# Kernel tuning notes

Measured on AMD Instinct MI355X. Metric: run time of the kernel, lower is better.

The kernel has to match this reference:

```python
import math
import jax, jax.numpy as jnp
import numpy as np

B, S, H, NH = 2, 2048, 1024, 16
HD = H // NH
SQRT7 = math.sqrt(7.0)


def bitlinear(x, W, scale):
    # ternary weight quant: round(W / mean|W|) clipped to [-1,1], rescaled
    w_mean = jnp.mean(jnp.abs(W))
    w_q = jnp.clip(jnp.round(W / (w_mean + 1e-5)), -1.0, 1.0)
    return x @ (w_q * w_mean * scale).T


def int4_quant(x):
    beta = jnp.mean(jnp.abs(x), axis=-1, keepdims=True)
    scale = beta * SQRT7
    x_q = jnp.clip(jnp.round(x * SQRT7 / (beta + 1e-5)), -8.0, 7.0)
    return x_q * scale / SQRT7


def int8_quant(x):
    gamma = jnp.max(jnp.abs(x), axis=-1, keepdims=True)
    x_q = jnp.clip(jnp.round(x * 127.0 / (gamma + 1e-5)), -128.0, 127.0)
    return x_q * gamma / 127.0


def topk_sparsify(x, k_frac=0.5):
    abs_x = jnp.abs(x)
    num_keep = int(k_frac * x.shape[-1])
    # torch.kthvalue(k=num_keep) -> num_keep-th smallest (1-indexed)
    sorted_abs = jnp.sort(abs_x, axis=-1)
    threshold = sorted_abs[..., num_keep - 1:num_keep]
    mask = (abs_x >= threshold).astype(x.dtype)
    return x * mask


def setup_inputs() -> dict:
    key = jax.random.key(0)
    ks = jax.random.split(key, 5)
    inp = {
        "hidden_states": jax.random.normal(ks[0], (B, S, H), dtype=jnp.float32),
        "Wq": jax.random.normal(ks[1], (H, H), dtype=jnp.float32) * (1.0 / math.sqrt(H)),
        "Wk": jax.random.normal(ks[2], (H, H), dtype=jnp.float32) * (1.0 / math.sqrt(H)),
        "Wv": jax.random.normal(ks[3], (H, H), dtype=jnp.float32) * (1.0 / math.sqrt(H)),
        "Wo": jax.random.normal(ks[4], (H, H), dtype=jnp.float32) * (1.0 / math.sqrt(H)),
        "sq": jnp.ones((1,), dtype=jnp.float32),
        "sk": jnp.ones((1,), dtype=jnp.float32),
        "sv": jnp.ones((1,), dtype=jnp.float32),
        "so": jnp.ones((1,), dtype=jnp.float32),
    }
    return inp


def reference(hidden_states, Wq, Wk, Wv, Wo, sq, sk, sv, so):
    x = int4_quant(hidden_states)                      # [B,S,H]
    q = bitlinear(x, Wq, sq).reshape(B, S, NH, HD)
    k = bitlinear(x, Wk, sk).reshape(B, S, NH, HD)
    v = bitlinear(x, Wv, sv).reshape(B, S, NH, HD)
    scores = jnp.einsum("bqhd,bkhd->bhqk", q, k) / math.sqrt(HD)
    probs = jax.nn.softmax(scores, axis=-1)
    ctx = jnp.einsum("bhqk,bkhd->bqhd", probs, v).reshape(B, S, H)
    ctx = int8_quant(ctx)
    ctx = topk_sparsify(ctx, 0.5)
    return bitlinear(ctx, Wo, so)
```

## Files before the change

### kernel.cpp

```cpp
#include <hip/hip_runtime.h>
#include <math.h>

#define NTOK 4096
#define HDIM 1024
#define NHEADS 16
#define HD 64
#define SEQ 2048
#define WSZ (HDIM*HDIM)
#define NM (NTOK*HDIM)
#define SQ7F 2.6457513110645906f
#define KC_BLK 384


__global__ __launch_bounds__(1024) void k_wmean_s1(const float* __restrict__ Wq,
                                                   const float* __restrict__ Wk,
                                                   const float* __restrict__ Wv,
                                                   const float* __restrict__ Wo,
                                                   float* __restrict__ bsG) {
  int w = blockIdx.y;
  const float* W = (w == 0) ? Wq : (w == 1) ? Wk : (w == 2) ? Wv : Wo;
  int idx = blockIdx.x * 1024 + threadIdx.x;
  const float* a = W + (size_t)idx * 128;
  float4 f0 = *(const float4*)(a);
  float4 f1 = *(const float4*)(a + 4);
  float r0 = fabsf(f0.x), r1 = fabsf(f0.y), r2 = fabsf(f0.z), r3 = fabsf(f0.w);
  float r4 = fabsf(f1.x), r5 = fabsf(f1.y), r6 = fabsf(f1.z), r7 = fabsf(f1.w);
#pragma unroll
  for (int g = 1; g < 16; g++) {
    float4 g0 = *(const float4*)(a + g * 8);
    float4 g1 = *(const float4*)(a + g * 8 + 4);
    r0 = __fadd_rn(r0, fabsf(g0.x)); r1 = __fadd_rn(r1, fabsf(g0.y));
    r2 = __fadd_rn(r2, fabsf(g0.z)); r3 = __fadd_rn(r3, fabsf(g0.w));
    r4 = __fadd_rn(r4, fabsf(g1.x)); r5 = __fadd_rn(r5, fabsf(g1.y));
    r6 = __fadd_rn(r6, fabsf(g1.z)); r7 = __fadd_rn(r7, fabsf(g1.w));
  }
  bsG[w * 8192 + idx] = __fadd_rn(__fadd_rn(__fadd_rn(r0, r1), __fadd_rn(r2, r3)),
                                  __fadd_rn(__fadd_rn(r4, r5), __fadd_rn(r6, r7)));
}

__global__ __launch_bounds__(1024) void k_wmean_s2(const float* __restrict__ bsG,
                                                   float* __restrict__ wm4) {
  __shared__ float bsA[8192];
  __shared__ float bsB[4096];
  int w = blockIdx.x, t = threadIdx.x;
  for (int i = t; i < 8192; i += 1024) bsA[i] = bsG[w * 8192 + i];
  __syncthreads();
  float* cur = bsA;
  float* nxt = bsB;
  for (int len = 4096; len >= 1; len >>= 1) {
    for (int i = t; i < len; i += 1024)
      nxt[i] = __fadd_rn(cur[2 * i], cur[2 * i + 1]);
    __syncthreads();
    float* tmp = cur; cur = nxt; nxt = tmp;
  }
  if (t == 0) wm4[w] = cur[0] / 1048576.0f;
}

__global__ void k_wquant_np(const float* __restrict__ Wq, const float* __restrict__ Wk,
                            const float* __restrict__ Wv, const float* __restrict__ Wo,
                            const float* __restrict__ wm4, float* __restrict__ M,
                            const float* __restrict__ sq, const float* __restrict__ sk,
                            const float* __restrict__ sv, const float* __restrict__ so) {
  int w = blockIdx.y;
  const float* W = (w == 0) ? Wq : (w == 1) ? Wk : (w == 2) ? Wv : Wo;
  float s = (w == 0) ? sq[0] : (w == 1) ? sk[0] : (w == 2) ? sv[0] : so[0];
  float wm = wm4[w];
  float wme = __fadd_rn(wm, 1e-5f);
  int i = blockIdx.x * 1024 + threadIdx.x * 4;
  float4 v = *(const float4*)(W + i);
  float4 o;
  o.x = __fmul_rn(__fmul_rn(fminf(fmaxf(rintf(__fdiv_rn(v.x, wme)), -1.f), 1.f), wm), s);
  o.y = __fmul_rn(__fmul_rn(fminf(fmaxf(rintf(__fdiv_rn(v.y, wme)), -1.f), 1.f), wm), s);
  o.z = __fmul_rn(__fmul_rn(fminf(fmaxf(rintf(__fdiv_rn(v.z, wme)), -1.f), 1.f), wm), s);
  o.w = __fmul_rn(__fmul_rn(fminf(fmaxf(rintf(__fdiv_rn(v.w, wme)), -1.f), 1.f), wm), s);
  *(float4*)(M + (size_t)w * WSZ + i) = o;
}

__global__ __launch_bounds__(256) void k_xquant_np(const float* __restrict__ x,
                                                   float* __restrict__ xd) {
  int t = threadIdx.x, wave = t >> 6, lane = t & 63;
  int n = blockIdx.x * 4 + wave;
  const float* row = x + (size_t)n * HDIM;
  int b = lane >> 3, j = lane & 7;
  const float* ch = row + b * 128 + j;
  float acc = fabsf(ch[0]);
#pragma unroll
  for (int i = 1; i < 16; i++) acc = __fadd_rn(acc, fabsf(ch[i * 8]));
  int gb = lane & ~7;
  float r0 = __shfl(acc, gb + 0), r1 = __shfl(acc, gb + 1),
        r2 = __shfl(acc, gb + 2), r3 = __shfl(acc, gb + 3),
        r4 = __shfl(acc, gb + 4), r5 = __shfl(acc, gb + 5),
        r6 = __shfl(acc, gb + 6), r7 = __shfl(acc, gb + 7);
  float bsum = __fadd_rn(__fadd_rn(__fadd_rn(r0, r1), __fadd_rn(r2, r3)),
                         __fadd_rn(__fadd_rn(r4, r5), __fadd_rn(r6, r7)));
  float b0 = __shfl(bsum, 0),  b1 = __shfl(bsum, 8),  b2 = __shfl(bsum, 16),
        b3 = __shfl(bsum, 24), b4 = __shfl(bsum, 32), b5 = __shfl(bsum, 40),
        b6 = __shfl(bsum, 48), b7 = __shfl(bsum, 56);
  float total = __fadd_rn(__fadd_rn(__fadd_rn(b0, b1), __fadd_rn(b2, b3)),
                          __fadd_rn(__fadd_rn(b4, b5), __fadd_rn(b6, b7)));
  float beta = total / 1024.0f;
  float bpe = __fadd_rn(beta, 1e-5f);
  float scale = __fmul_rn(beta, SQ7F);
  float* od = xd + (size_t)n * HDIM;
#pragma unroll
  for (int i = 0; i < 4; i++) {
    float4 v = *(const float4*)(row + i * 256 + lane * 4);
    float4 o;
    o.x = __fdiv_rn(__fmul_rn(fminf(fmaxf(rintf(__fdiv_rn(__fmul_rn(v.x, SQ7F), bpe)), -8.f), 7.f), scale), SQ7F);
    o.y = __fdiv_rn(__fmul_rn(fminf(fmaxf(rintf(__fdiv_rn(__fmul_rn(v.y, SQ7F), bpe)), -8.f), 7.f), scale), SQ7F);
    o.z = __fdiv_rn(__fmul_rn(fminf(fmaxf(rintf(__fdiv_rn(__fmul_rn(v.z, SQ7F), bpe)), -8.f), 7.f), scale), SQ7F);
    o.w = __fdiv_rn(__fmul_rn(fminf(fmaxf(rintf(__fdiv_rn(__fmul_rn(v.w, SQ7F), bpe)), -8.f), 7.f), scale), SQ7F);
    *(float4*)(od + i * 256 + lane * 4) = o;
  }
}

__global__ __launch_bounds__(256) void k_gemm_blas(const float* __restrict__ A,
                                                   const float* __restrict__ Bm,
                                                   float* __restrict__ C) {
  __shared__ __align__(16) float As[16 * 68];
  __shared__ __align__(16) float Bs[16 * 68];
  int t = threadIdx.x;
  int o0 = blockIdx.x * 64, n0 = blockIdx.y * 64;
  int lr = t >> 2, lc = (t & 3) * 4;
  const float* Ag = A + (size_t)(n0 + lr) * HDIM + lc;
  const float* Bg = Bm + (size_t)(o0 + lr) * HDIM + lc;
  int tn = (t & 15) * 4, to = (t >> 4) * 4;
  float acc[4][4] = {};
  float accP[4][4] = {};
  for (int kt = 0; kt < HDIM; kt += 16) {
    if (kt == KC_BLK || kt == 2 * KC_BLK) {
#pragma unroll
      for (int i = 0; i < 4; i++)
#pragma unroll
        for (int j = 0; j < 4; j++) {
          accP[i][j] = __fadd_rn(accP[i][j], acc[i][j]);
          acc[i][j] = 0.f;
        }
    }
    float4 a = *(const float4*)(Ag + kt);
    float4 b = *(const float4*)(Bg + kt);
    __syncthreads();
    float av[4] = {a.x, a.y, a.z, a.w};
    float bv[4] = {b.x, b.y, b.z, b.w};
#pragma unroll
    for (int u = 0; u < 4; u++) {
      As[(lc + u) * 68 + lr] = av[u];
      Bs[(lc + u) * 68 + lr] = bv[u];
    }
    __syncthreads();
#pragma unroll
    for (int kc = 0; kc < 16; kc++) {
      float4 a4 = *(const float4*)&As[kc * 68 + tn];
      float4 b4 = *(const float4*)&Bs[kc * 68 + to];
      float aa[4] = {a4.x, a4.y, a4.z, a4.w};
      float bb[4] = {b4.x, b4.y, b4.z, b4.w};
#pragma unroll
      for (int i = 0; i < 4; i++)
#pragma unroll
        for (int j = 0; j < 4; j++)
          acc[i][j] = __fmaf_rn(aa[i], bb[j], acc[i][j]);
    }
  }
#pragma unroll
  for (int i = 0; i < 4; i++) {
    float4 v;
    v.x = __fadd_rn(accP[i][0], acc[i][0]);
    v.y = __fadd_rn(accP[i][1], acc[i][1]);
    v.z = __fadd_rn(accP[i][2], acc[i][2]);
    v.w = __fadd_rn(accP[i][3], acc[i][3]);
    *(float4*)(C + (size_t)(n0 + tn + i) * HDIM + o0 + to) = v;
  }
}

__global__ __launch_bounds__(256, 3) void k_attn_np(const float* __restrict__ qb,
                                                    const float* __restrict__ kb,
                                                    const float* __restrict__ vb,
                                                    float* __restrict__ ctx) {
  __shared__ __align__(16) float Ks[64 * 68];
  __shared__ __align__(16) float Vs[64 * 68];
  int bh = blockIdx.y;
  int b = bh >> 4, h = bh & 15;
  int t = threadIdx.x, wave = t >> 6, lane = t & 63;
  int r0 = blockIdx.x * 8 + wave * 2;
  size_t base = (size_t)b * SEQ * HDIM + h * HD;
  const float* qg0 = qb + base + (size_t)r0 * HDIM;
  const float* qg1 = qg0 + HDIM;

  int tok = t >> 2, dpar = t & 3;
  int th = lane >> 5, tk = lane & 31;
  int off = th * 32;
  int rA = tk * 68 + off, rB = (tk + 32) * 68 + off;

  float o0[32], o1[32];
#pragma unroll
  for (int j = 0; j < 32; j++) { o0[j] = 0.f; o1[j] = 0.f; }
  float m0 = -INFINITY, m1 = -INFINITY;
  float S0 = 0.f, S1 = 0.f;

  for (int c = 0; c < 32; c++) {
    int j0 = c * 64;
    __syncthreads();
    {
      const float* kg = kb + base + (size_t)(j0 + tok) * HDIM + dpar * 4;
      const float* vg = vb + base + (size_t)(j0 + tok) * HDIM + dpar * 4;
      float* kd = &Ks[tok * 68 + dpar * 4];
      float* vd = &Vs[tok * 68 + dpar * 4];
#pragma unroll
      for (int u = 0; u < 4; u++) {
        *(float4*)(kd + u * 16) = *(const float4*)(kg + u * 16);
        *(float4*)(vd + u * 16) = *(const float4*)(vg + u * 16);
      }
    }
    __syncthreads();

    float dA0 = 0.f, dB0 = 0.f, dA1 = 0.f, dB1 = 0.f;
#pragma unroll
    for (int i = 0; i < 8; i++) {
      float4 kA = *(const float4*)&Ks[rA + i * 4];
      float4 kB = *(const float4*)&Ks[rB + i * 4];
      float4 q0 = *(const float4*)(qg0 + off + i * 4);
      float4 q1 = *(const float4*)(qg1 + off + i * 4);
      dA0 = __fmaf_rn(q0.x, kA.x, dA0); dA0 = __fmaf_rn(q0.y, kA.y, dA0);
      dA0 = __fmaf_rn(q0.z, kA.z, dA0); dA0 = __fmaf_rn(q0.w, kA.w, dA0);
      dB0 = __fmaf_rn(q0.x, kB.x, dB0); dB0 = __fmaf_rn(q0.y, kB.y, dB0);
      dB0 = __fmaf_rn(q0.z, kB.z, dB0); dB0 = __fmaf_rn(q0.w, kB.w, dB0);
      dA1 = __fmaf_rn(q1.x, kA.x, dA1); dA1 = __fmaf_rn(q1.y, kA.y, dA1);
      dA1 = __fmaf_rn(q1.z, kA.z, dA1); dA1 = __fmaf_rn(q1.w, kA.w, dA1);
      dB1 = __fmaf_rn(q1.x, kB.x, dB1); dB1 = __fmaf_rn(q1.y, kB.y, dB1);
      dB1 = __fmaf_rn(q1.z, kB.z, dB1); dB1 = __fmaf_rn(q1.w, kB.w, dB1);
    }
    float sA0 = __fmul_rn(__fadd_rn(dA0, __shfl_xor(dA0, 32)), 0.125f);
    float sB0 = __fmul_rn(__fadd_rn(dB0, __shfl_xor(dB0, 32)), 0.125f);
    float sA1 = __fmul_rn(__fadd_rn(dA1, __shfl_xor(dA1, 32)), 0.125f);
    float sB1 = __fmul_rn(__fadd_rn(dB1, __shfl_xor(dB1, 32)), 0.125f);

    float cm0 = fmaxf(sA0, sB0);
#pragma unroll
    for (int o = 16; o; o >>= 1) cm0 = fmaxf(cm0, __shfl_xor(cm0, o));
    if (cm0 > m0) {
      float f = expf(m0 - cm0);
      S0 = __fmul_rn(S0, f);
#pragma unroll
      for (int j = 0; j < 32; j++) o0[j] = __fmul_rn(o0[j], f);
      m0 = cm0;
    }
    float pA0 = expf(__fadd_rn(sA0, -m0));
    float pB0 = expf(__fadd_rn(sB0, -m0));
    S0 = __fadd_rn(S0, __fadd_rn(pA0, pB0));

    float cm1 = fmaxf(sA1, sB1);
#pragma unroll
    for (int o = 16; o; o >>= 1) cm1 = fmaxf(cm1, __shfl_xor(cm1, o));
    if (cm1 > m1) {
      float f = expf(m1 - cm1);
      S1 = __fmul_rn(S1, f);
#pragma unroll
      for (int j = 0; j < 32; j++) o1[j] = __fmul_rn(o1[j], f);
      m1 = cm1;
    }
    float pA1 = expf(__fadd_rn(sA1, -m1));
    float pB1 = expf(__fadd_rn(sB1, -m1));
    S1 = __fadd_rn(S1, __fadd_rn(pA1, pB1));

#pragma unroll
    for (int i = 0; i < 8; i++) {
      float4 vA = *(const float4*)&Vs[rA + i * 4];
      float4 vB = *(const float4*)&Vs[rB + i * 4];
      o0[i * 4 + 0] = __fmaf_rn(pB0, vB.x, __fmaf_rn(pA0, vA.x, o0[i * 4 + 0]));
      o0[i * 4 + 1] = __fmaf_rn(pB0, vB.y, __fmaf_rn(pA0, vA.y, o0[i * 4 + 1]));
      o0[i * 4 + 2] = __fmaf_rn(pB0, vB.z, __fmaf_rn(pA0, vA.z, o0[i * 4 + 2]));
      o0[i * 4 + 3] = __fmaf_rn(pB0, vB.w, __fmaf_rn(pA0, vA.w, o0[i * 4 + 3]));
      o1[i * 4 + 0] = __fmaf_rn(pB1, vB.x, __fmaf_rn(pA1, vA.x, o1[i * 4 + 0]));
      o1[i * 4 + 1] = __fmaf_rn(pB1, vB.y, __fmaf_rn(pA1, vA.y, o1[i * 4 + 1]));
      o1[i * 4 + 2] = __fmaf_rn(pB1, vB.z, __fmaf_rn(pA1, vA.z, o1[i * 4 + 2]));
      o1[i * 4 + 3] = __fmaf_rn(pB1, vB.w, __fmaf_rn(pA1, vA.w, o1[i * 4 + 3]));
    }
  }

#pragma unroll
  for (int o = 16; o; o >>= 1) S0 = __fadd_rn(S0, __shfl_xor(S0, o));
#pragma unroll
  for (int o = 16; o; o >>= 1) S1 = __fadd_rn(S1, __shfl_xor(S1, o));

  __syncthreads();
  float* Osw = ((wave < 2) ? Ks : Vs) + (wave & 1) * 2176;
  int dd = lane, thd = dd >> 5, jd = dd & 31;
  size_t cb = base + (size_t)r0 * HDIM;
#pragma unroll
  for (int j = 0; j < 32; j++) Osw[lane * 33 + j] = o0[j];
  float a0 = Osw[(thd * 32 + 0) * 33 + jd];
#pragma unroll
  for (int s = 1; s < 32; s++) a0 = __fadd_rn(a0, Osw[(thd * 32 + s) * 33 + jd]);
  ctx[cb + dd] = __fdiv_rn(a0, S0);
#pragma unroll
  for (int j = 0; j < 32; j++) Osw[lane * 33 + j] = o1[j];
  float a1 = Osw[(thd * 32 + 0) * 33 + jd];
#pragma unroll
  for (int s = 1; s < 32; s++) a1 = __fadd_rn(a1, Osw[(thd * 32 + s) * 33 + jd]);
  ctx[cb + HDIM + dd] = __fdiv_rn(a1, S1);
}

__global__ __launch_bounds__(256) void k_ctxq_np(const float* __restrict__ ctx,
                                                 float* __restrict__ cqm) {
  int n = blockIdx.x, t = threadIdx.x;
  __shared__ float red[256];
  __shared__ int hist[129];
  __shared__ int tsh;
  float4 cv = *(const float4*)(ctx + (size_t)n * HDIM + t * 4);
  float mx = fmaxf(fmaxf(fabsf(cv.x), fabsf(cv.y)), fmaxf(fabsf(cv.z), fabsf(cv.w)));
  red[t] = mx; __syncthreads();
  for (int st = 128; st > 0; st >>= 1) {
    if (t < st) red[t] = fmaxf(red[t], red[t + st]);
    __syncthreads();
  }
  float gamma = red[0];
  if (t < 129) hist[t] = 0;
  __syncthreads();
  float gpe = __fadd_rn(gamma, 1e-5f);
  float q0 = fminf(fmaxf(rintf(__fdiv_rn(__fmul_rn(cv.x, 127.0f), gpe)), -128.f), 127.f);
  float q1 = fminf(fmaxf(rintf(__fdiv_rn(__fmul_rn(cv.y, 127.0f), gpe)), -128.f), 127.f);
  float q2 = fminf(fmaxf(rintf(__fdiv_rn(__fmul_rn(cv.z, 127.0f), gpe)), -128.f), 127.f);
  float q3 = fminf(fmaxf(rintf(__fdiv_rn(__fmul_rn(cv.w, 127.0f), gpe)), -128.f), 127.f);
  int a0 = (int)fabsf(q0), a1 = (int)fabsf(q1), a2 = (int)fabsf(q2), a3 = (int)fabsf(q3);
  atomicAdd(&hist[a0], 1); atomicAdd(&hist[a1], 1);
  atomicAdd(&hist[a2], 1); atomicAdd(&hist[a3], 1);
  __syncthreads();
  if (t < 129) {
    int cum = 0;
    for (int u = 0; u <= t; u++) cum += hist[u];
    if (cum >= 512 && cum - hist[t] < 512) tsh = t;
  }
  __syncthreads();
  int thr = tsh;
  float4 o;
  o.x = (a0 >= thr) ? __fdiv_rn(__fmul_rn(q0, gamma), 127.0f) : 0.f;
  o.y = (a1 >= thr) ? __fdiv_rn(__fmul_rn(q1, gamma), 127.0f) : 0.f;
  o.z = (a2 >= thr) ? __fdiv_rn(__fmul_rn(q2, gamma), 127.0f) : 0.f;
  o.w = (a3 >= thr) ? __fdiv_rn(__fmul_rn(q3, gamma), 127.0f) : 0.f;
  *(float4*)(cqm + (size_t)n * HDIM + t * 4) = o;
}

extern "C" void kernel_launch(void* const* d_in, const int* in_sizes, int n_in,
                              void* d_out, int out_size, void* d_ws, size_t ws_size,
                              hipStream_t stream) {
  const float* x  = (const float*)d_in[0];
  const float* Wq = (const float*)d_in[1];
  const float* Wk = (const float*)d_in[2];
  const float* Wv = (const float*)d_in[3];
  const float* Wo = (const float*)d_in[4];
  const float* sq = (const float*)d_in[5];
  const float* sk = (const float*)d_in[6];
  const float* sv = (const float*)d_in[7];
  const float* so = (const float*)d_in[8];
  float* out = (float*)d_out;

  float* F   = (float*)d_ws;
  float* wm4 = F;
  float* M   = F + 1024;
  float* XD  = M + (size_t)4 * WSZ;
  float* Q   = XD + (size_t)NM;
  float* K   = Q + (size_t)NM;
  float* V   = K + (size_t)NM;
  float* ctx = XD;
  float* cqm = Q;

  k_wmean_s1<<<dim3(8, 4), 1024, 0, stream>>>(Wq, Wk, Wv, Wo, M);
  k_wmean_s2<<<4, 1024, 0, stream>>>(M, wm4);
  k_wquant_np<<<dim3(1024, 4), 256, 0, stream>>>(Wq, Wk, Wv, Wo, wm4, M, sq, sk, sv, so);
  k_xquant_np<<<1024, 256, 0, stream>>>(x, XD);

  k_gemm_blas<<<dim3(16, 64), 256, 0, stream>>>(XD, M + 0 * (size_t)WSZ, Q);
  k_gemm_blas<<<dim3(16, 64), 256, 0, stream>>>(XD, M + 1 * (size_t)WSZ, K);
  k_gemm_blas<<<dim3(16, 64), 256, 0, stream>>>(XD, M + 2 * (size_t)WSZ, V);

  k_attn_np<<<dim3(256, 32), 256, 0, stream>>>(Q, K, V, ctx);

  k_ctxq_np<<<4096, 256, 0, stream>>>(ctx, cqm);

  k_gemm_blas<<<dim3(16, 64), 256, 0, stream>>>(cqm, M + 3 * (size_t)WSZ, out);
}
```

Baseline: 1.852 ms.

## Double-buffer attention K/V tiles with direct global-to-LDS loads and XOR swizzle

```diff
diff --git a/kernel.cpp b/kernel.cpp
--- a/kernel.cpp
+++ b/kernel.cpp
@@ -11,6 +11,12 @@
 #define SQ7F 2.6457513110645906f
 #define KC_BLK 384
 
+
+__device__ __forceinline__ void gload_lds16(const float* g, float* l) {
+  __builtin_amdgcn_global_load_lds(
+      (const __attribute__((address_space(1))) void*)g,
+      (__attribute__((address_space(3))) void*)l, 16, 0, 0);
+}
 
 __global__ __launch_bounds__(1024) void k_wmean_s1(const float* __restrict__ Wq,
                                                    const float* __restrict__ Wk,
@@ -172,12 +178,12 @@
   }
 }
 
-__global__ __launch_bounds__(256, 3) void k_attn_np(const float* __restrict__ qb,
+__global__ __launch_bounds__(256, 2) void k_attn_np(const float* __restrict__ qb,
                                                     const float* __restrict__ kb,
                                                     const float* __restrict__ vb,
                                                     float* __restrict__ ctx) {
-  __shared__ __align__(16) float Ks[64 * 68];
-  __shared__ __align__(16) float Vs[64 * 68];
+  __shared__ __align__(16) float Ks2[2][64 * 64];
+  __shared__ __align__(16) float Vs2[2][64 * 64];
   int bh = blockIdx.y;
   int b = bh >> 4, h = bh & 15;
   int t = threadIdx.x, wave = t >> 6, lane = t & 63;
@@ -186,10 +192,13 @@
   const float* qg0 = qb + base + (size_t)r0 * HDIM;
   const float* qg1 = qg0 + HDIM;
 
-  int tok = t >> 2, dpar = t & 3;
+  int lrow = lane >> 4, lgr = lane & 15;
+  int rbase = wave << 4;
+
   int th = lane >> 5, tk = lane & 31;
-  int off = th * 32;
-  int rA = tk * 68 + off, rB = (tk + 32) * 68 + off;
+  int th8 = th * 8;
+  int sxA = tk & 15;
+  int rA = tk * 64, rB = (tk + 32) * 64;
 
   float o0[32], o1[32];
 #pragma unroll
@@ -197,29 +206,44 @@
   float m0 = -INFINITY, m1 = -INFINITY;
   float S0 = 0.f, S1 = 0.f;
 
+#pragma unroll
+  for (int u = 0; u < 4; u++) {
+    int row = rbase + u * 4 + lrow;
+    int g = lgr ^ (row & 15);
+    const float* gk = kb + base + (size_t)row * HDIM + g * 4;
+    const float* gv = vb + base + (size_t)row * HDIM + g * 4;
+    gload_lds16(gk, &Ks2[0][(rbase + u * 4) * 64]);
+    gload_lds16(gv, &Vs2[0][(rbase + u * 4) * 64]);
+  }
+  __syncthreads();
+
   for (int c = 0; c < 32; c++) {
-    int j0 = c * 64;
-    __syncthreads();
-    {
-      const float* kg = kb + base + (size_t)(j0 + tok) * HDIM + dpar * 4;
-      const float* vg = vb + base + (size_t)(j0 + tok) * HDIM + dpar * 4;
-      float* kd = &Ks[tok * 68 + dpar * 4];
-      float* vd = &Vs[tok * 68 + dpar * 4];
+    int cur = c & 1;
+    if (c < 31) {
+      int nb = cur ^ 1;
+      size_t goff = base + (size_t)(c + 1) * 64 * HDIM;
 #pragma unroll
       for (int u = 0; u < 4; u++) {
-        *(float4*)(kd + u * 16) = *(const float4*)(kg + u * 16);
-        *(float4*)(vd + u * 16) = *(const float4*)(vg + u * 16);
+        int row = rbase + u * 4 + lrow;
+        int g = lgr ^ (row & 15);
+        const float* gk = kb + goff + (size_t)row * HDIM + g * 4;
+        const float* gv = vb + goff + (size_t)row * HDIM + g * 4;
+        gload_lds16(gk, &Ks2[nb][(rbase + u * 4) * 64]);
+        gload_lds16(gv, &Vs2[nb][(rbase + u * 4) * 64]);
       }
     }
-    __syncthreads();
+
+    const float* Kb = &Ks2[cur][0];
+    const float* Vb = &Vs2[cur][0];
 
     float dA0 = 0.f, dB0 = 0.f, dA1 = 0.f, dB1 = 0.f;
 #pragma unroll
     for (int i = 0; i < 8; i++) {
-      float4 kA = *(const float4*)&Ks[rA + i * 4];
-      float4 kB = *(const float4*)&Ks[rB + i * 4];
-      float4 q0 = *(const float4*)(qg0 + off + i * 4);
-      float4 q1 = *(const float4*)(qg1 + off + i * 4);
+      int p4 = ((th8 + i) ^ sxA) * 4;
+      float4 kA = *(const float4*)&Kb[rA + p4];
+      float4 kB = *(const float4*)&Kb[rB + p4];
+      float4 q0 = *(const float4*)(qg0 + th8 * 4 + i * 4);
+      float4 q1 = *(const float4*)(qg1 + th8 * 4 + i * 4);
       dA0 = __fmaf_rn(q0.x, kA.x, dA0); dA0 = __fmaf_rn(q0.y, kA.y, dA0);
       dA0 = __fmaf_rn(q0.z, kA.z, dA0); dA0 = __fmaf_rn(q0.w, kA.w, dA0);
       dB0 = __fmaf_rn(q0.x, kB.x, dB0); dB0 = __fmaf_rn(q0.y, kB.y, dB0);
@@ -264,8 +288,9 @@
 
 #pragma unroll
     for (int i = 0; i < 8; i++) {
-      float4 vA = *(const float4*)&Vs[rA + i * 4];
-      float4 vB = *(const float4*)&Vs[rB + i * 4];
+      int p4 = ((th8 + i) ^ sxA) * 4;
+      float4 vA = *(const float4*)&Vb[rA + p4];
+      float4 vB = *(const float4*)&Vb[rB + p4];
       o0[i * 4 + 0] = __fmaf_rn(pB0, vB.x, __fmaf_rn(pA0, vA.x, o0[i * 4 + 0]));
       o0[i * 4 + 1] = __fmaf_rn(pB0, vB.y, __fmaf_rn(pA0, vA.y, o0[i * 4 + 1]));
       o0[i * 4 + 2] = __fmaf_rn(pB0, vB.z, __fmaf_rn(pA0, vA.z, o0[i * 4 + 2]));
@@ -275,6 +300,8 @@
       o1[i * 4 + 2] = __fmaf_rn(pB1, vB.z, __fmaf_rn(pA1, vA.z, o1[i * 4 + 2]));
       o1[i * 4 + 3] = __fmaf_rn(pB1, vB.w, __fmaf_rn(pA1, vA.w, o1[i * 4 + 3]));
     }
+
+    __syncthreads();
   }
 
 #pragma unroll
@@ -282,22 +309,21 @@
 #pragma unroll
   for (int o = 16; o; o >>= 1) S1 = __fadd_rn(S1, __shfl_xor(S1, o));
 
-  __syncthreads();
-  float* Osw = ((wave < 2) ? Ks : Vs) + (wave & 1) * 2176;
-  int dd = lane, thd = dd >> 5, jd = dd & 31;
+  float* Osw = ((wave < 2) ? &Ks2[0][0] : &Vs2[0][0]) + (wave & 1) * 2112;
+  int thd = lane >> 5, jd = lane & 31;
   size_t cb = base + (size_t)r0 * HDIM;
 #pragma unroll
   for (int j = 0; j < 32; j++) Osw[lane * 33 + j] = o0[j];
   float a0 = Osw[(thd * 32 + 0) * 33 + jd];
 #pragma unroll
   for (int s = 1; s < 32; s++) a0 = __fadd_rn(a0, Osw[(thd * 32 + s) * 33 + jd]);
-  ctx[cb + dd] = __fdiv_rn(a0, S0);
+  ctx[cb + lane] = __fdiv_rn(a0, S0);
 #pragma unroll
   for (int j = 0; j < 32; j++) Osw[lane * 33 + j] = o1[j];
   float a1 = Osw[(thd * 32 + 0) * 33 + jd];
 #pragma unroll
   for (int s = 1; s < 32; s++) a1 = __fadd_rn(a1, Osw[(thd * 32 + s) * 33 + jd]);
-  ctx[cb + HDIM + dd] = __fdiv_rn(a1, S1);
+  ctx[cb + HDIM + lane] = __fdiv_rn(a1, S1);
 }
 
 __global__ __launch_bounds__(256) void k_ctxq_np(const float* __restrict__ ctx,
```

After: 1.629 ms. 12.1% less time.
